# Optimization experiments

Measured on AMD Instinct MI355X. Metric: run time of the kernel, lower is better.

## Reference

```python
import math
import jax, jax.numpy as jnp
import numpy as np

B, T_BI, D_BI = 64, 3000, 128
T_SW, D_SW = 375, 192
T_S1, D_S1 = 188, 192
N_FIRES = 300          # static fire count (target_lengths all = 300 -> beta = 1, ceil(sum)=300)
D_MODEL = 512
SCALE = 4.0            # scale_factor
EPS_LN = 1e-5


def _cif_integrate(h, alpha, thr, n_fires):
    """Vectorized CIF: cumsum + two scatter-adds (matches torch _cif_forward).
    h [B,T,D], alpha [B,T], thr [B,1] -> [B,n_fires,D]."""
    Bq, T, D = h.shape
    a = alpha / thr                       # normalize so boundaries sit at integers
    c = jnp.cumsum(a, axis=1)
    prev = c - a
    kp = jnp.floor(prev)
    kc = jnp.floor(c)
    fired = kc > kp                       # frame crosses a token boundary
    w_hi = jnp.where(fired, (c - kc) * thr, 0.0)          # leftover into new token
    w_lo = jnp.where(fired, (kp + 1.0 - prev) * thr, alpha)  # portion completing old token
    ip = jnp.clip(kp.astype(jnp.int32), 0, n_fires - 1)
    ic = jnp.clip(kc.astype(jnp.int32), 0, n_fires - 1)
    bidx = jnp.broadcast_to(jnp.arange(Bq)[:, None], (Bq, T))
    out = jnp.zeros((Bq, n_fires, D), h.dtype)
    out = out.at[bidx, ip].add(w_lo[..., None] * h)
    out = out.at[bidx, ic].add(w_hi[..., None] * h)
    return out


def _interp(src, t_cont, t_bi):
    """Linear interp of src [B,Ts,D] at continuous fire times t_cont [B,N] (given on the T_bi grid)."""
    Bq, Ts, D = src.shape
    t = t_cont * Ts / t_bi
    lo = jnp.clip(t.astype(jnp.int32), 0, Ts - 2)
    w = (t - lo.astype(t.dtype))[..., None]
    idx_lo = jnp.broadcast_to(lo[..., None], (Bq, t.shape[1], D))
    g_lo = jnp.take_along_axis(src, idx_lo, axis=1)
    g_hi = jnp.take_along_axis(src, idx_lo + 1, axis=1)
    return (1.0 - w) * g_lo + w * g_hi


def _forward(fire_signal, acoustic_src, acoustic_src_s1, conv_w, ln_g, ln_b, wp_w, wp_b,
             film_s0_w, film_s0_b, film_s1_w, film_s1_b, tproj_w, tproj_b,
             aproj_w, aproj_b, bproj_w, bproj_b, target_lengths):
    Bq, T_bi, _ = fire_signal.shape
    # 1) weight predictor: depthwise conv (k=1, no bias) -> LN -> Linear -> sigmoid
    x = fire_signal * conv_w                                   # depthwise 1x1 conv
    mu = jnp.mean(x, axis=-1, keepdims=True)
    var = jnp.var(x, axis=-1, keepdims=True)
    xn = (x - mu) * jax.lax.rsqrt(var + EPS_LN) * ln_g + ln_b
    alpha = SCALE * jax.nn.sigmoid(xn @ wp_w + wp_b)           # [B,T]
    tgt = target_lengths.astype(alpha.dtype)
    qty_loss = jnp.mean(jnp.abs(jnp.sum(alpha, axis=1) - tgt))
    # training-mode alpha normalization (sum alpha_cif == target)
    sum_a = jnp.clip(jnp.sum(alpha, axis=1, keepdims=True), 1e-8)
    alpha_cif = alpha * (tgt[:, None] / sum_a)
    # dynamic threshold beta = sum / ceil(sum)  (== 1 here since targets are integers)
    sum_cif = jnp.sum(alpha_cif, axis=1)
    ceil_sum = jax.lax.stop_gradient(jnp.clip(jnp.ceil(sum_cif), 1.0))
    thr = (sum_cif / ceil_sum)[:, None]                        # [B,1]
    # 2) CIF integration of temporal channel
    acoustic_temporal = _cif_integrate(fire_signal, alpha_cif, thr, N_FIRES)  # [B,N,128]
    # continuous fire times
    cum = jnp.cumsum(alpha_cif, axis=1)
    thresholds = jnp.arange(1, N_FIRES + 1, dtype=alpha.dtype)[None, :] * thr  # [B,N]
    ff = jax.vmap(jnp.searchsorted)(cum, thresholds)
    ff = jnp.minimum(ff, T_bi - 1)
    t_lo = jnp.maximum(ff - 1, 0)
    cum_at = jnp.take_along_axis(cum, t_lo, axis=1)
    a_at = jnp.take_along_axis(alpha_cif, ff, axis=1)
    t_cont = t_lo.astype(alpha.dtype) + (thresholds - cum_at) / jnp.clip(a_at, 1e-8)
    t_cont = jnp.clip(t_cont, 0.0, T_bi - 1)
    # 3) S0 pitch channel: interp + FiLM
    acoustic_pitch = _interp(acoustic_src, t_cont, T_bi)       # [B,N,192]
    film0 = acoustic_temporal @ film_s0_w + film_s0_b
    g0, b0 = jnp.split(film0, 2, axis=-1)
    pitch_mod = g0 * acoustic_pitch + b0
    # 4) project + combine
    embs = (acoustic_temporal @ tproj_w + tproj_b) + (pitch_mod @ aproj_w + aproj_b)
    # S1 beat channel
    acoustic_beat = _interp(acoustic_src_s1, t_cont, T_bi)     # [B,N,192]
    film1 = acoustic_temporal @ film_s1_w + film_s1_b
    g1, b1 = jnp.split(film1, 2, axis=-1)
    beat_mod = g1 * acoustic_beat + b1
    embs = embs + (beat_mod @ bproj_w + bproj_b)
    return embs, alpha, qty_loss


def setup_inputs() -> dict:
    key = jax.random.key(0)
    ks = jax.random.split(key, 14)
    # weight_proj bias init per module: alpha_init = target_fires/encoder_len
    p = min((128.0 / 3000.0) / SCALE, 0.99)
    wp_bias = math.log(p / (1.0 - p))
    f32 = jnp.float32
    return {
        "fire_signal": jax.random.normal(ks[0], (B, T_BI, D_BI), f32),
        "acoustic_src": jax.random.normal(ks[1], (B, T_SW, D_SW), f32),
        "acoustic_src_s1": jax.random.normal(ks[2], (B, T_S1, D_S1), f32),
        "target_lengths": jnp.full((B,), N_FIRES, jnp.int32),
        "conv_w": 1.0 + 0.1 * jax.random.normal(ks[3], (D_BI,), f32),
        "ln_g": jnp.ones((D_BI,), f32),
        "ln_b": jnp.zeros((D_BI,), f32),
        "wp_w": 0.02 * jax.random.normal(ks[4], (D_BI,), f32),
        "wp_b": jnp.asarray(wp_bias, f32),
        "film_s0_w": 0.02 * jax.random.normal(ks[5], (D_BI, 2 * D_SW), f32),
        "film_s0_b": jnp.concatenate([jnp.ones((D_SW,), f32), jnp.zeros((D_SW,), f32)]),
        "film_s1_w": 0.02 * jax.random.normal(ks[6], (D_BI, 2 * D_S1), f32),
        "film_s1_b": jnp.concatenate([jnp.ones((D_S1,), f32), jnp.zeros((D_S1,), f32)]),
        "tproj_w": 0.02 * jax.random.normal(ks[7], (D_BI, D_MODEL), f32),
        "tproj_b": jnp.zeros((D_MODEL,), f32),
        "aproj_w": 0.02 * jax.random.normal(ks[8], (D_SW, D_MODEL), f32),
        "aproj_b": jnp.zeros((D_MODEL,), f32),
        "bproj_w": 0.02 * jax.random.normal(ks[9], (D_S1, D_MODEL), f32),
        "bproj_b": jnp.zeros((D_MODEL,), f32),
    }


def reference(fire_signal, acoustic_src, acoustic_src_s1, target_lengths, conv_w, ln_g, ln_b,
              wp_w, wp_b, film_s0_w, film_s0_b, film_s1_w, film_s1_b, tproj_w, tproj_b,
              aproj_w, aproj_b, bproj_w, bproj_b):
    return _forward(fire_signal, acoustic_src, acoustic_src_s1, conv_w, ln_g, ln_b, wp_w, wp_b,
                    film_s0_w, film_s0_b, film_s1_w, film_s1_b, tproj_w, tproj_b,
                    aproj_w, aproj_b, bproj_w, bproj_b, target_lengths)
```

## Files before the change

### kernel.cpp

```cpp
#include <hip/hip_runtime.h>
#include <math.h>

#define BQ 64
#define TBI 3000
#define DBI 128
#define TSW 375
#define TS1 188
#define DSW 192
#define NF 300
#define DMODEL 512
#define EPSLN 1e-5f

typedef __bf16 bf16x8 __attribute__((ext_vector_type(8)));
typedef float f32x4 __attribute__((ext_vector_type(4)));

__device__ __forceinline__ unsigned short f2bf(float f) {
    unsigned u = __float_as_uint(f);
    unsigned r = (u + 0x7FFFu + ((u >> 16) & 1u)) >> 16;
    return (unsigned short)r;
}

__global__ __launch_bounds__(256) void k_alpha2(
    const float* __restrict__ fs, const float* __restrict__ conv_w,
    const float* __restrict__ ln_g, const float* __restrict__ ln_b,
    const float* __restrict__ wp_w, const float* __restrict__ wp_b,
    float* __restrict__ alpha_out)
{
    int wave = threadIdx.x >> 6, lane = threadIdx.x & 63;
    int l = lane & 31;
    long g = (long)blockIdx.x * 8 + wave * 2 + (lane >> 5);
    const float* row = fs + g * DBI;
    float4 f  = *(const float4*)&row[4 * l];
    float4 cw = *(const float4*)&conv_w[4 * l];
    float4 x; x.x = f.x * cw.x; x.y = f.y * cw.y; x.z = f.z * cw.z; x.w = f.w * cw.w;
    float s = x.x + x.y + x.z + x.w;
    for (int m = 16; m >= 1; m >>= 1) s += __shfl_xor(s, m, 64);
    float mu = s * (1.0f / 128.0f);
    float4 d; d.x = x.x - mu; d.y = x.y - mu; d.z = x.z - mu; d.w = x.w - mu;
    float q = d.x * d.x + d.y * d.y + d.z * d.z + d.w * d.w;
    for (int m = 16; m >= 1; m >>= 1) q += __shfl_xor(q, m, 64);
    float var = q * (1.0f / 128.0f);
    float rs = rsqrtf(var + EPSLN);
    float4 lg = *(const float4*)&ln_g[4 * l];
    float4 lb = *(const float4*)&ln_b[4 * l];
    float4 wp = *(const float4*)&wp_w[4 * l];
    float z = (d.x * rs * lg.x + lb.x) * wp.x + (d.y * rs * lg.y + lb.y) * wp.y
            + (d.z * rs * lg.z + lb.z) * wp.z + (d.w * rs * lg.w + lb.w) * wp.w;
    for (int m = 16; m >= 1; m >>= 1) z += __shfl_xor(z, m, 64);
    z += wp_b[0];
    float a = 4.0f / (1.0f + expf(-z));
    if (l == 0) alpha_out[g] = a;
}

__global__ __launch_bounds__(1024) void k_scan3(
    const float* __restrict__ alpha, const int* __restrict__ tlen,
    float2* __restrict__ params, float* __restrict__ qtyo,
    float2* __restrict__ c2, float* __restrict__ tcont, int* __restrict__ ffout)
{
    __shared__ float2 sc[TBI];
    __shared__ float2 part[2][1024];
    __shared__ double red[1024];
    int b = blockIdx.x, tid = threadIdx.x;
    const float* ar = alpha + (long)b * TBI;
    double s = 0.0;
    for (int t = tid; t < TBI; t += 1024) s += (double)ar[t];
    red[tid] = s; __syncthreads();
    for (int d = 512; d >= 1; d >>= 1) { if (tid < d) red[tid] += red[tid + d]; __syncthreads(); }
    double sum_a = red[0]; __syncthreads();
    double tgt = (double)tlen[b];
    double sa = sum_a < 1e-8 ? 1e-8 : sum_a;
    float r = (float)(tgt / sa);
    double s2 = 0.0;
    for (int t = tid; t < TBI; t += 1024) s2 += (double)(ar[t] * r);
    red[tid] = s2; __syncthreads();
    for (int d = 512; d >= 1; d >>= 1) { if (tid < d) red[tid] += red[tid + d]; __syncthreads(); }
    float sum_cif = (float)red[0];
    float cs = ceilf(sum_cif); if (cs < 1.0f) cs = 1.0f;
    float thr = sum_cif / cs;
    float rthr = 1.0f / thr;
    if (tid == 0) {
        params[b] = make_float2(r, thr);
        atomicAdd(qtyo, (float)fabs(sum_a - tgt) * (1.0f / (float)BQ));
    }
    int base = tid * 3;
    float2 run = make_float2(0.f, 0.f);
    if (base < TBI) {
        for (int j = 0; j < 3; ++j) {
            int t = base + j;
            float ac = ar[t] * r;
            run.x += ac * rthr; run.y += ac;
            sc[t] = run;
        }
    }
    part[0][tid] = (base < TBI) ? run : make_float2(0.f, 0.f);
    __syncthreads();
    int srcb = 0;
    for (int d = 1; d < 1024; d <<= 1) {
        float2 v = part[srcb][tid];
        if (tid >= d) { float2 u = part[srcb][tid - d]; v.x += u.x; v.y += u.y; }
        part[srcb ^ 1][tid] = v;
        srcb ^= 1;
        __syncthreads();
    }
    if (base < TBI && tid > 0) {
        float2 off = part[srcb][tid - 1];
        for (int j = 0; j < 3; ++j) { sc[base + j].x += off.x; sc[base + j].y += off.y; }
    }
    __syncthreads();
    for (int t = tid; t < TBI; t += 1024) {
        float ac = ar[t] * r;
        c2[(long)b * TBI + t] = make_float2(sc[t].x, ac);
    }
    if (tid < NF) {
        float v = (float)(tid + 1) * thr;
        int lo = 0, hi = TBI;
        while (lo < hi) { int mid = (lo + hi) >> 1; if (sc[mid].y < v) lo = mid + 1; else hi = mid; }
        int ff = lo; if (ff > TBI - 1) ff = TBI - 1;
        ffout[b * NF + tid] = ff;
        int tl = ff - 1; if (tl < 0) tl = 0;
        float cum_at = sc[tl].y;
        float a_at = ar[ff] * r;
        if (a_at < 1e-8f) a_at = 1e-8f;
        float tc = (float)tl + (v - cum_at) / a_at;
        tc = fminf(fmaxf(tc, 0.0f), (float)(TBI - 1));
        tcont[b * NF + tid] = tc;
    }
}

#define TPW 3
__global__ __launch_bounds__(256) void k_cif3(
    const float* __restrict__ fs, const float2* __restrict__ c2,
    const int* __restrict__ ffA, const float2* __restrict__ params,
    float* __restrict__ at)
{
    int wid = threadIdx.x >> 6, lane = threadIdx.x & 63;
    int wg = blockIdx.x * 4 + wid;
    int b = wg / 100, slot = wg - b * 100;
    int j0 = slot * TPW;
    const int* ffb = ffA + b * NF;
    int t0 = (j0 == 0) ? 0 : ffb[j0 - 1];
    int tE = (slot == 99) ? (TBI - 1) : ffb[j0 + TPW - 1];
    float thr = params[b].y;
    float rthr = 1.0f / thr;
    const float2* cb = c2 + (long)b * TBI;
    const float* fb = fs + (long)b * TBI * DBI;
    float* ab = at + (long)b * NF * DBI;
    int nw = j0;
    int cur = -1;
    float a0 = 0.f, a1 = 0.f;
    #define FLUSH() do { \
        if (cur >= j0 && cur < j0 + TPW) { \
            while (nw < cur) { *(float2*)&ab[nw * DBI + 2 * lane] = make_float2(0.f, 0.f); ++nw; } \
            *(float2*)&ab[cur * DBI + 2 * lane] = make_float2(a0, a1); nw = cur + 1; \
        } } while (0)
    for (int t = t0; t <= tE; ++t) {
        float2 v = cb[t];
        float2 h = *(const float2*)&fb[(long)t * DBI + 2 * lane];
        float c = v.x, ac = v.y;
        float av = ac * rthr;
        float prev = c - av;
        float kp = floorf(prev), kc = floorf(c);
        bool fired = kc > kp;
        float w_lo = fired ? (kp + 1.0f - prev) * thr : ac;
        float w_hi = fired ? (c - kc) * thr : 0.0f;
        int ip = (int)kp; if (ip > NF - 1) ip = NF - 1; if (ip < 0) ip = 0;
        int ic = (int)kc; if (ic > NF - 1) ic = NF - 1; if (ic < 0) ic = 0;
        if (ip != cur) { FLUSH(); cur = ip; a0 = 0.f; a1 = 0.f; }
        a0 += w_lo * h.x; a1 += w_lo * h.y;
        if (fired) {
            if (ic != cur) { FLUSH(); cur = ic; a0 = 0.f; a1 = 0.f; }
            a0 += w_hi * h.x; a1 += w_hi * h.y;
        }
    }
    FLUSH();
    while (nw < j0 + TPW) { *(float2*)&ab[nw * DBI + 2 * lane] = make_float2(0.f, 0.f); ++nw; }
    #undef FLUSH
}

__global__ __launch_bounds__(256) void k_prep2(
    const float* __restrict__ f0w, const float* __restrict__ f1w,
    const float* __restrict__ tw, const float* __restrict__ aw, const float* __restrict__ bw,
    const float* __restrict__ f0b, const float* __restrict__ f1b,
    const float* __restrict__ tb, const float* __restrict__ apb, const float* __restrict__ bpb,
    unsigned short* __restrict__ Wg, unsigned short* __restrict__ Wb,
    unsigned short* __restrict__ W2,
    float* __restrict__ gbias, float* __restrict__ bbias, float* __restrict__ bias2,
    float* __restrict__ qtyo)
{
    if (blockIdx.x == 1216) {
        for (int c = threadIdx.x; c < 512; c += 256) {
            if (c < 384) {
                gbias[c] = c < 192 ? f0b[c] : f1b[c - 192];
                bbias[c] = c < 192 ? f0b[c + 192] : f1b[c - 192 + 192];
            }
            bias2[c] = tb[c] + apb[c] + bpb[c];
        }
        if (threadIdx.x == 0) qtyo[0] = 0.f;
        return;
    }
    int i = blockIdx.x * 256 + threadIdx.x;
    if (i < 49152) {
        int j = i & 7, lane = (i >> 3) & 63, kt = (i >> 9) & 3, nt = i >> 11;
        int k = kt * 32 + (lane >> 4) * 8 + j;
        int n = nt * 16 + (lane & 15);
        float g, b;
        if (n < 192) { g = f0w[k * 384 + n];         b = f0w[k * 384 + n + 192]; }
        else         { g = f1w[k * 384 + (n - 192)]; b = f1w[k * 384 + (n - 192) + 192]; }
        Wg[i] = f2bf(g); Wb[i] = f2bf(b);
    } else {
        int ii = i - 49152;
        int j = ii & 7, lane = (ii >> 3) & 63, kt = (ii >> 9) & 15, nt = ii >> 13;
        int k = kt * 32 + (lane >> 4) * 8 + j;
        int n = nt * 16 + (lane & 15);
        float v;
        if (k < 128)      v = tw[k * 512 + n];
        else if (k < 320) v = aw[(k - 128) * 512 + n];
        else              v = bw[(k - 320) * 512 + n];
        W2[ii] = f2bf(v);
    }
}

#define EROWS 16
__global__ __launch_bounds__(512, 6) void k_emb5(
    const float* __restrict__ at, const float* __restrict__ tcont,
    const float* __restrict__ src0, const float* __restrict__ src1,
    const unsigned short* __restrict__ Wg, const unsigned short* __restrict__ Wb,
    const unsigned short* __restrict__ W2,
    const float* __restrict__ gbias, const float* __restrict__ bbias,
    const float* __restrict__ bias2, float* __restrict__ embs)
{
    __shared__ __align__(16) unsigned short X[EROWS][520];
    __shared__ float s_w0[EROWS], s_w1[EROWS];
    __shared__ int s_lo0[EROWS], s_lo1[EROWS], s_b[EROWS];
    int tid = threadIdx.x;
    int wave = tid >> 6, lane = tid & 63;
    long r0 = (long)blockIdx.x * EROWS;
    {
        int r = tid >> 5, k4 = (tid & 31) * 4;
        float4 v = *(const float4*)&at[(r0 + r) * DBI + k4];
        X[r][k4 + 0] = f2bf(v.x); X[r][k4 + 1] = f2bf(v.y);
        X[r][k4 + 2] = f2bf(v.z); X[r][k4 + 3] = f2bf(v.w);
    }
    if (tid < EROWS) {
        long g = r0 + tid;
        s_b[tid] = (int)(g / NF);
        float tc = tcont[g];
        float t0 = tc * ((float)TSW / 3000.0f);
        int lo0 = (int)t0; if (lo0 > TSW - 2) lo0 = TSW - 2; if (lo0 < 0) lo0 = 0;
        s_lo0[tid] = lo0; s_w0[tid] = t0 - (float)lo0;
        float t1 = tc * ((float)TS1 / 3000.0f);
        int lo1 = (int)t1; if (lo1 > TS1 - 2) lo1 = TS1 - 2; if (lo1 < 0) lo1 = 0;
        s_lo1[tid] = lo1; s_w1[tid] = t1 - (float)lo1;
    }
    __syncthreads();
    int mrow = lane & 15, quad = lane >> 4;
    for (int nt = wave; nt < 24; nt += 8) {
        f32x4 ag = {0,0,0,0}, ab = {0,0,0,0};
        #pragma unroll
        for (int kt = 0; kt < 4; ++kt) {
            bf16x8 a = *(const bf16x8*)&X[mrow][kt * 32 + quad * 8];
            bf16x8 bg = *(const bf16x8*)&Wg[(((nt * 4 + kt) * 64) + lane) * 8];
            bf16x8 bb = *(const bf16x8*)&Wb[(((nt * 4 + kt) * 64) + lane) * 8];
            ag = __builtin_amdgcn_mfma_f32_16x16x32_bf16(a, bg, ag, 0, 0, 0);
            ab = __builtin_amdgcn_mfma_f32_16x16x32_bf16(a, bb, ab, 0, 0, 0);
        }
        int c = nt * 16 + mrow;
        bool sel = c >= DSW;
        int cc = sel ? c - DSW : c;
        const float* S = sel ? src1 : src0;
        int Ts = sel ? TS1 : TSW;
        float gb = gbias[c], bbv = bbias[c];
        #pragma unroll
        for (int q = 0; q < 4; ++q) {
            int r = quad * 4 + q;
            int b = s_b[r];
            int lo = sel ? s_lo1[r] : s_lo0[r];
            float w = sel ? s_w1[r] : s_w0[r];
            const float* Sp = S + ((long)b * Ts + lo) * DSW + cc;
            float pv = (1.0f - w) * Sp[0] + w * Sp[DSW];
            X[r][128 + c] = f2bf((ag[q] + gb) * pv + (ab[q] + bbv));
        }
    }
    __syncthreads();
    f32x4 acc[4];
    #pragma unroll
    for (int n = 0; n < 4; ++n) acc[n] = (f32x4){0, 0, 0, 0};
    for (int kt = 0; kt < 16; ++kt) {
        bf16x8 a = *(const bf16x8*)&X[mrow][kt * 32 + quad * 8];
        #pragma unroll
        for (int n = 0; n < 4; ++n) {
            int nt = wave * 4 + n;
            bf16x8 bfv = *(const bf16x8*)&W2[((nt * 16 + kt) * 64 + lane) * 8];
            acc[n] = __builtin_amdgcn_mfma_f32_16x16x32_bf16(a, bfv, acc[n], 0, 0, 0);
        }
    }
    #pragma unroll
    for (int n = 0; n < 4; ++n) {
        int cbase = (wave * 4 + n) * 16 + mrow;
        float bv = bias2[cbase];
        #pragma unroll
        for (int q = 0; q < 4; ++q)
            embs[(r0 + quad * 4 + q) * DMODEL + cbase] = acc[n][q] + bv;
    }
}

extern "C" void kernel_launch(void* const* d_in, const int* in_sizes, int n_in,
                              void* d_out, int out_size, void* d_ws, size_t ws_size,
                              hipStream_t stream)
{
    const float* fs     = (const float*)d_in[0];
    const float* src0   = (const float*)d_in[1];
    const float* src1   = (const float*)d_in[2];
    const int*   tlen   = (const int*)d_in[3];
    const float* conv_w = (const float*)d_in[4];
    const float* ln_g   = (const float*)d_in[5];
    const float* ln_b   = (const float*)d_in[6];
    const float* wp_w   = (const float*)d_in[7];
    const float* wp_b   = (const float*)d_in[8];
    const float* f0w    = (const float*)d_in[9];
    const float* f0b    = (const float*)d_in[10];
    const float* f1w    = (const float*)d_in[11];
    const float* f1b    = (const float*)d_in[12];
    const float* tw     = (const float*)d_in[13];
    const float* tb     = (const float*)d_in[14];
    const float* aw     = (const float*)d_in[15];
    const float* apb    = (const float*)d_in[16];
    const float* bw     = (const float*)d_in[17];
    const float* bpb    = (const float*)d_in[18];

    float* embs  = (float*)d_out;
    float* alpha = embs + (long)BQ * NF * DMODEL;
    float* qtyo  = alpha + (long)BQ * TBI;

    char* ws = (char*)d_ws;
    size_t off = 0;
    float*  at     = (float*)(ws + off);  off += 9830400;
    float2* c2     = (float2*)(ws + off); off += 1536000;
    float*  tcont  = (float*)(ws + off);  off += 76800;
    int*    ffA    = (int*)(ws + off);    off += 76800;
    float2* params = (float2*)(ws + off); off += 512;
    unsigned short* Wg = (unsigned short*)(ws + off); off += 98304;
    unsigned short* Wb = (unsigned short*)(ws + off); off += 98304;
    unsigned short* W2 = (unsigned short*)(ws + off); off += 524288;
    float* gbias = (float*)(ws + off); off += 1536;
    float* bbias = (float*)(ws + off); off += 1536;
    float* bias2 = (float*)(ws + off); off += 2048;

    k_prep2<<<1217, 256, 0, stream>>>(f0w, f1w, tw, aw, bw, f0b, f1b, tb, apb, bpb,
                                      Wg, Wb, W2, gbias, bbias, bias2, qtyo);
    k_alpha2<<<(BQ * TBI) / 8, 256, 0, stream>>>(fs, conv_w, ln_g, ln_b, wp_w, wp_b, alpha);
    k_scan3<<<BQ, 1024, 0, stream>>>(alpha, tlen, params, qtyo, c2, tcont, ffA);
    k_cif3<<<(BQ * 100) / 4, 256, 0, stream>>>(fs, c2, ffA, params, at);
    k_emb5<<<(BQ * NF) / EROWS, 512, 0, stream>>>(at, tcont, src0, src1,
                                                  Wg, Wb, W2, gbias, bbias, bias2, embs);
}
```

Measured before the change: 276.5 us.

## Fuse weight prep into alpha kernel, store CIF output as bf16, double emb rows

Merges the weight-packing prep kernel into the alpha-predictor launch as extra trailing blocks, which removes one kernel launch. The CIF integrator now writes its accumulated rows directly as bf16, halving the intermediate buffer traffic and letting the embedding kernel copy them without converting. The embedding kernel processes 32 rows per block, so each weight fragment load feeds two MFMAs. That raises register and LDS use and lowers the occupancy hint.

```diff
diff --git a/kernel.cpp b/kernel.cpp
--- a/kernel.cpp
+++ b/kernel.cpp
@@ -20,12 +20,57 @@
     return (unsigned short)r;
 }
 
-__global__ __launch_bounds__(256) void k_alpha2(
+#define ALPHA_BLOCKS 24000
+
+__global__ __launch_bounds__(256) void k_alpha_prep(
     const float* __restrict__ fs, const float* __restrict__ conv_w,
     const float* __restrict__ ln_g, const float* __restrict__ ln_b,
     const float* __restrict__ wp_w, const float* __restrict__ wp_b,
-    float* __restrict__ alpha_out)
-{
+    float* __restrict__ alpha_out,
+    const float* __restrict__ f0w, const float* __restrict__ f1w,
+    const float* __restrict__ tw, const float* __restrict__ aw, const float* __restrict__ bw,
+    const float* __restrict__ f0b, const float* __restrict__ f1b,
+    const float* __restrict__ tb, const float* __restrict__ apb, const float* __restrict__ bpb,
+    unsigned short* __restrict__ Wg, unsigned short* __restrict__ Wb,
+    unsigned short* __restrict__ W2,
+    float* __restrict__ gbias, float* __restrict__ bbias, float* __restrict__ bias2,
+    float* __restrict__ qtyo)
+{
+    if (blockIdx.x >= ALPHA_BLOCKS) {
+        int pbid = blockIdx.x - ALPHA_BLOCKS;
+        if (pbid == 1216) {
+            for (int c = threadIdx.x; c < 512; c += 256) {
+                if (c < 384) {
+                    gbias[c] = c < 192 ? f0b[c] : f1b[c - 192];
+                    bbias[c] = c < 192 ? f0b[c + 192] : f1b[c - 192 + 192];
+                }
+                bias2[c] = tb[c] + apb[c] + bpb[c];
+            }
+            if (threadIdx.x == 0) qtyo[0] = 0.f;
+            return;
+        }
+        int i = pbid * 256 + threadIdx.x;
+        if (i < 49152) {
+            int j = i & 7, lane = (i >> 3) & 63, kt = (i >> 9) & 3, nt = i >> 11;
+            int k = kt * 32 + (lane >> 4) * 8 + j;
+            int n = nt * 16 + (lane & 15);
+            float g, b;
+            if (n < 192) { g = f0w[k * 384 + n];         b = f0w[k * 384 + n + 192]; }
+            else         { g = f1w[k * 384 + (n - 192)]; b = f1w[k * 384 + (n - 192) + 192]; }
+            Wg[i] = f2bf(g); Wb[i] = f2bf(b);
+        } else {
+            int ii = i - 49152;
+            int j = ii & 7, lane = (ii >> 3) & 63, kt = (ii >> 9) & 15, nt = ii >> 13;
+            int k = kt * 32 + (lane >> 4) * 8 + j;
+            int n = nt * 16 + (lane & 15);
+            float v;
+            if (k < 128)      v = tw[k * 512 + n];
+            else if (k < 320) v = aw[(k - 128) * 512 + n];
+            else              v = bw[(k - 320) * 512 + n];
+            W2[ii] = f2bf(v);
+        }
+        return;
+    }
     int wave = threadIdx.x >> 6, lane = threadIdx.x & 63;
     int l = lane & 31;
     long g = (long)blockIdx.x * 8 + wave * 2 + (lane >> 5);
@@ -131,7 +176,7 @@
 __global__ __launch_bounds__(256) void k_cif3(
     const float* __restrict__ fs, const float2* __restrict__ c2,
     const int* __restrict__ ffA, const float2* __restrict__ params,
-    float* __restrict__ at)
+    unsigned short* __restrict__ at)
 {
     int wid = threadIdx.x >> 6, lane = threadIdx.x & 63;
     int wg = blockIdx.x * 4 + wid;
@@ -144,14 +189,14 @@
     float rthr = 1.0f / thr;
     const float2* cb = c2 + (long)b * TBI;
     const float* fb = fs + (long)b * TBI * DBI;
-    float* ab = at + (long)b * NF * DBI;
+    unsigned short* ab = at + (long)b * NF * DBI;
     int nw = j0;
     int cur = -1;
     float a0 = 0.f, a1 = 0.f;
     #define FLUSH() do { \
         if (cur >= j0 && cur < j0 + TPW) { \
-            while (nw < cur) { *(float2*)&ab[nw * DBI + 2 * lane] = make_float2(0.f, 0.f); ++nw; } \
-            *(float2*)&ab[cur * DBI + 2 * lane] = make_float2(a0, a1); nw = cur + 1; \
+            while (nw < cur) { *(unsigned*)&ab[nw * DBI + 2 * lane] = 0u; ++nw; } \
+            *(unsigned*)&ab[cur * DBI + 2 * lane] = (unsigned)f2bf(a0) | ((unsigned)f2bf(a1) << 16); nw = cur + 1; \
         } } while (0)
     for (int t = t0; t <= tE; ++t) {
         float2 v = cb[t];
@@ -173,56 +218,13 @@
         }
     }
     FLUSH();
-    while (nw < j0 + TPW) { *(float2*)&ab[nw * DBI + 2 * lane] = make_float2(0.f, 0.f); ++nw; }
+    while (nw < j0 + TPW) { *(unsigned*)&ab[nw * DBI + 2 * lane] = 0u; ++nw; }
     #undef FLUSH
 }
 
-__global__ __launch_bounds__(256) void k_prep2(
-    const float* __restrict__ f0w, const float* __restrict__ f1w,
-    const float* __restrict__ tw, const float* __restrict__ aw, const float* __restrict__ bw,
-    const float* __restrict__ f0b, const float* __restrict__ f1b,
-    const float* __restrict__ tb, const float* __restrict__ apb, const float* __restrict__ bpb,
-    unsigned short* __restrict__ Wg, unsigned short* __restrict__ Wb,
-    unsigned short* __restrict__ W2,
-    float* __restrict__ gbias, float* __restrict__ bbias, float* __restrict__ bias2,
-    float* __restrict__ qtyo)
-{
-    if (blockIdx.x == 1216) {
-        for (int c = threadIdx.x; c < 512; c += 256) {
-            if (c < 384) {
-                gbias[c] = c < 192 ? f0b[c] : f1b[c - 192];
-                bbias[c] = c < 192 ? f0b[c + 192] : f1b[c - 192 + 192];
-            }
-            bias2[c] = tb[c] + apb[c] + bpb[c];
-        }
-        if (threadIdx.x == 0) qtyo[0] = 0.f;
-        return;
-    }
-    int i = blockIdx.x * 256 + threadIdx.x;
-    if (i < 49152) {
-        int j = i & 7, lane = (i >> 3) & 63, kt = (i >> 9) & 3, nt = i >> 11;
-        int k = kt * 32 + (lane >> 4) * 8 + j;
-        int n = nt * 16 + (lane & 15);
-        float g, b;
-        if (n < 192) { g = f0w[k * 384 + n];         b = f0w[k * 384 + n + 192]; }
-        else         { g = f1w[k * 384 + (n - 192)]; b = f1w[k * 384 + (n - 192) + 192]; }
-        Wg[i] = f2bf(g); Wb[i] = f2bf(b);
-    } else {
-        int ii = i - 49152;
-        int j = ii & 7, lane = (ii >> 3) & 63, kt = (ii >> 9) & 15, nt = ii >> 13;
-        int k = kt * 32 + (lane >> 4) * 8 + j;
-        int n = nt * 16 + (lane & 15);
-        float v;
-        if (k < 128)      v = tw[k * 512 + n];
-        else if (k < 320) v = aw[(k - 128) * 512 + n];
-        else              v = bw[(k - 320) * 512 + n];
-        W2[ii] = f2bf(v);
-    }
-}
-
-#define EROWS 16
-__global__ __launch_bounds__(512, 6) void k_emb5(
-    const float* __restrict__ at, const float* __restrict__ tcont,
+#define EROWS 32
+__global__ __launch_bounds__(512, 4) void k_emb6(
+    const unsigned short* __restrict__ atb, const float* __restrict__ tcont,
     const float* __restrict__ src0, const float* __restrict__ src1,
     const unsigned short* __restrict__ Wg, const unsigned short* __restrict__ Wb,
     const unsigned short* __restrict__ W2,
@@ -236,10 +238,8 @@
     int wave = tid >> 6, lane = tid & 63;
     long r0 = (long)blockIdx.x * EROWS;
     {
-        int r = tid >> 5, k4 = (tid & 31) * 4;
-        float4 v = *(const float4*)&at[(r0 + r) * DBI + k4];
-        X[r][k4 + 0] = f2bf(v.x); X[r][k4 + 1] = f2bf(v.y);
-        X[r][k4 + 2] = f2bf(v.z); X[r][k4 + 3] = f2bf(v.w);
+        int r = tid >> 4, k8 = (tid & 15) * 8;
+        *(uint4*)&X[r][k8] = *(const uint4*)&atb[(r0 + r) * DBI + k8];
     }
     if (tid < EROWS) {
         long g = r0 + tid;
@@ -255,14 +255,17 @@
     __syncthreads();
     int mrow = lane & 15, quad = lane >> 4;
     for (int nt = wave; nt < 24; nt += 8) {
-        f32x4 ag = {0,0,0,0}, ab = {0,0,0,0};
+        f32x4 ag0 = {0,0,0,0}, ab0 = {0,0,0,0}, ag1 = {0,0,0,0}, ab1 = {0,0,0,0};
         #pragma unroll
         for (int kt = 0; kt < 4; ++kt) {
-            bf16x8 a = *(const bf16x8*)&X[mrow][kt * 32 + quad * 8];
+            bf16x8 a0 = *(const bf16x8*)&X[mrow][kt * 32 + quad * 8];
+            bf16x8 a1 = *(const bf16x8*)&X[mrow + 16][kt * 32 + quad * 8];
             bf16x8 bg = *(const bf16x8*)&Wg[(((nt * 4 + kt) * 64) + lane) * 8];
             bf16x8 bb = *(const bf16x8*)&Wb[(((nt * 4 + kt) * 64) + lane) * 8];
-            ag = __builtin_amdgcn_mfma_f32_16x16x32_bf16(a, bg, ag, 0, 0, 0);
-            ab = __builtin_amdgcn_mfma_f32_16x16x32_bf16(a, bb, ab, 0, 0, 0);
+            ag0 = __builtin_amdgcn_mfma_f32_16x16x32_bf16(a0, bg, ag0, 0, 0, 0);
+            ab0 = __builtin_amdgcn_mfma_f32_16x16x32_bf16(a0, bb, ab0, 0, 0, 0);
+            ag1 = __builtin_amdgcn_mfma_f32_16x16x32_bf16(a1, bg, ag1, 0, 0, 0);
+            ab1 = __builtin_amdgcn_mfma_f32_16x16x32_bf16(a1, bb, ab1, 0, 0, 0);
         }
         int c = nt * 16 + mrow;
         bool sel = c >= DSW;
@@ -272,26 +275,41 @@
         float gb = gbias[c], bbv = bbias[c];
         #pragma unroll
         for (int q = 0; q < 4; ++q) {
-            int r = quad * 4 + q;
-            int b = s_b[r];
-            int lo = sel ? s_lo1[r] : s_lo0[r];
-            float w = sel ? s_w1[r] : s_w0[r];
-            const float* Sp = S + ((long)b * Ts + lo) * DSW + cc;
-            float pv = (1.0f - w) * Sp[0] + w * Sp[DSW];
-            X[r][128 + c] = f2bf((ag[q] + gb) * pv + (ab[q] + bbv));
+            {
+                int r = quad * 4 + q;
+                int b = s_b[r];
+                int lo = sel ? s_lo1[r] : s_lo0[r];
+                float w = sel ? s_w1[r] : s_w0[r];
+                const float* Sp = S + ((long)b * Ts + lo) * DSW + cc;
+                float pv = (1.0f - w) * Sp[0] + w * Sp[DSW];
+                X[r][128 + c] = f2bf((ag0[q] + gb) * pv + (ab0[q] + bbv));
+            }
+            {
+                int r = quad * 4 + q + 16;
+                int b = s_b[r];
+                int lo = sel ? s_lo1[r] : s_lo0[r];
+                float w = sel ? s_w1[r] : s_w0[r];
+                const float* Sp = S + ((long)b * Ts + lo) * DSW + cc;
+                float pv = (1.0f - w) * Sp[0] + w * Sp[DSW];
+                X[r][128 + c] = f2bf((ag1[q] + gb) * pv + (ab1[q] + bbv));
+            }
         }
     }
     __syncthreads();
-    f32x4 acc[4];
+    f32x4 acc[2][4];
     #pragma unroll
-    for (int n = 0; n < 4; ++n) acc[n] = (f32x4){0, 0, 0, 0};
+    for (int h = 0; h < 2; ++h)
+        #pragma unroll
+        for (int n = 0; n < 4; ++n) acc[h][n] = (f32x4){0, 0, 0, 0};
     for (int kt = 0; kt < 16; ++kt) {
-        bf16x8 a = *(const bf16x8*)&X[mrow][kt * 32 + quad * 8];
+        bf16x8 a0 = *(const bf16x8*)&X[mrow][kt * 32 + quad * 8];
+        bf16x8 a1 = *(const bf16x8*)&X[mrow + 16][kt * 32 + quad * 8];
         #pragma unroll
         for (int n = 0; n < 4; ++n) {
             int nt = wave * 4 + n;
             bf16x8 bfv = *(const bf16x8*)&W2[((nt * 16 + kt) * 64 + lane) * 8];
-            acc[n] = __builtin_amdgcn_mfma_f32_16x16x32_bf16(a, bfv, acc[n], 0, 0, 0);
+            acc[0][n] = __builtin_amdgcn_mfma_f32_16x16x32_bf16(a0, bfv, acc[0][n], 0, 0, 0);
+            acc[1][n] = __builtin_amdgcn_mfma_f32_16x16x32_bf16(a1, bfv, acc[1][n], 0, 0, 0);
         }
     }
     #pragma unroll
@@ -299,8 +317,10 @@
         int cbase = (wave * 4 + n) * 16 + mrow;
         float bv = bias2[cbase];
         #pragma unroll
-        for (int q = 0; q < 4; ++q)
-            embs[(r0 + quad * 4 + q) * DMODEL + cbase] = acc[n][q] + bv;
+        for (int q = 0; q < 4; ++q) {
+            embs[(r0 + quad * 4 + q) * DMODEL + cbase] = acc[0][n][q] + bv;
+            embs[(r0 + 16 + quad * 4 + q) * DMODEL + cbase] = acc[1][n][q] + bv;
+        }
     }
 }
 
@@ -334,7 +354,7 @@
 
     char* ws = (char*)d_ws;
     size_t off = 0;
-    float*  at     = (float*)(ws + off);  off += 9830400;
+    unsigned short* at = (unsigned short*)(ws + off); off += 4915200;
     float2* c2     = (float2*)(ws + off); off += 1536000;
     float*  tcont  = (float*)(ws + off);  off += 76800;
     int*    ffA    = (int*)(ws + off);    off += 76800;
@@ -346,11 +366,12 @@
     float* bbias = (float*)(ws + off); off += 1536;
     float* bias2 = (float*)(ws + off); off += 2048;
 
-    k_prep2<<<1217, 256, 0, stream>>>(f0w, f1w, tw, aw, bw, f0b, f1b, tb, apb, bpb,
-                                      Wg, Wb, W2, gbias, bbias, bias2, qtyo);
-    k_alpha2<<<(BQ * TBI) / 8, 256, 0, stream>>>(fs, conv_w, ln_g, ln_b, wp_w, wp_b, alpha);
+    k_alpha_prep<<<ALPHA_BLOCKS + 1217, 256, 0, stream>>>(
+        fs, conv_w, ln_g, ln_b, wp_w, wp_b, alpha,
+        f0w, f1w, tw, aw, bw, f0b, f1b, tb, apb, bpb,
+        Wg, Wb, W2, gbias, bbias, bias2, qtyo);
     k_scan3<<<BQ, 1024, 0, stream>>>(alpha, tlen, params, qtyo, c2, tcont, ffA);
     k_cif3<<<(BQ * 100) / 4, 256, 0, stream>>>(fs, c2, ffA, params, at);
-    k_emb5<<<(BQ * NF) / EROWS, 512, 0, stream>>>(at, tcont, src0, src1,
+    k_emb6<<<(BQ * NF) / EROWS, 512, 0, stream>>>(at, tcont, src0, src1,
                                                   Wg, Wb, W2, gbias, bbias, bias2, embs);
 }
```

Result: faster. 265.4 us (-4.0%).
